# Optimization experiments

Hardware: AMD Instinct MI355X
Metric: run time of the kernel (lower is better)

Reference implementation:

```python
import jax, jax.numpy as jnp
import numpy as np

N, K, D = 131072, 1024, 10


def setup_inputs() -> dict:
    key = jax.random.key(0)
    k1, k2 = jax.random.split(key)
    encoder_embedding = jax.random.normal(k1, (N, D), dtype=jnp.float32)
    embedding_weight = jax.random.normal(k2, (K, D), dtype=jnp.float32)
    return {"encoder_embedding": encoder_embedding, "embedding_weight": embedding_weight}


def reference(encoder_embedding, embedding_weight):
    x = encoder_embedding            # [N, D]
    E = embedding_weight             # [K, D]
    x_sq = jnp.sum(x * x, axis=1, keepdims=True)          # [N, 1]
    e_sq = jnp.sum(E * E, axis=1)                         # [K]
    distance = x_sq + e_sq - 2.0 * jnp.einsum('nd,kd->nk', x, E)
    idx = jnp.argmin(distance, axis=1)                    # [N]
    quantized = E[idx]                                    # [N, D] gather
    # codebook (quantization) loss: mse(x.detach(), quantized)
    diff = jax.lax.stop_gradient(x) - quantized
    quantization_loss = jnp.mean(diff * diff)
    # straight-through estimator
    quantized_st = x + jax.lax.stop_gradient(quantized - x)
    return (quantized_st, quantization_loss)
```

## Files before the change

kernel.cpp:

```cpp
#include <hip/hip_runtime.h>


typedef __attribute__((ext_vector_type(8))) short short8;
typedef __attribute__((ext_vector_type(16))) float f32x16;

constexpr int N = 131072;
constexpr int K = 1024;
constexpr int D = 10;
constexpr int TILES = 32;
constexpr int THREADS = 512;
constexpr int BLOCKS = 256;
constexpr int ROWS_PER_WAVE = 64;
constexpr int AFRAG_N = TILES * 3 * 64;
constexpr int SMEM_A_BYTES = AFRAG_N * 16;
constexpr int SMEM_B_PER_WAVE = ROWS_PER_WAVE * 96;
constexpr int SMEM_BYTES = SMEM_A_BYTES + 8 * SMEM_B_PER_WAVE;

__device__ float4 g_afrag[AFRAG_N];

__device__ inline unsigned short f2bf(float f) {
    unsigned u = __float_as_uint(f);
    u += 0x7FFFu + ((u >> 16) & 1u);
    return (unsigned short)(u >> 16);
}
__device__ inline float bf2f(unsigned short h) {
    return __uint_as_float(((unsigned)h) << 16);
}

__global__ __launch_bounds__(256) void prep_afrag(const float* __restrict__ E) {
    const int gid = blockIdx.x * blockDim.x + threadIdx.x;
    if (gid >= AFRAG_N) return;
    const int tile = gid / 192;
    const int rem  = gid % 192;
    const int v    = rem / 64;
    const int L    = rem % 64;
    const int code = tile * 32 + (L & 31);
    const int h    = L >> 5;

    float e[D];
    #pragma unroll
    for (int d = 0; d < D; ++d) e[d] = E[code * D + d];
    float s = 0.f;
    #pragma unroll
    for (int d = 0; d < D; ++d) s = fmaf(e[d], e[d], s);
    const float ms = -0.5f * s;
    const unsigned short msh = f2bf(ms);
    const float r1 = ms - bf2f(msh);
    const unsigned short msm = f2bf(r1);
    const unsigned short msl = f2bf(r1 - bf2f(msm));

    unsigned short sl[8];
    #pragma unroll
    for (int i = 0; i < 8; ++i) {
        const int k = h * 8 + i;
        unsigned short o = 0;
        if (k < D) {
            const unsigned short eh = f2bf(e[k]);
            if (v == 0) o = eh;
            else {
                const float rm = e[k] - bf2f(eh);
                const unsigned short em = f2bf(rm);
                o = (v == 1) ? em : f2bf(rm - bf2f(em));
            }
        } else if (v == 0) {
            o = (k == 10) ? msh : (k == 11) ? msm : (k == 12) ? msl : (unsigned short)0;
        }
        sl[i] = o;
    }
    float4 w;
    unsigned* wp = (unsigned*)&w;
    #pragma unroll
    for (int q = 0; q < 4; ++q)
        wp[q] = (unsigned)sl[2 * q] | ((unsigned)sl[2 * q + 1] << 16);
    g_afrag[gid] = w;
}

__global__ __launch_bounds__(THREADS, 2) void vq_kernel(
    const float* __restrict__ x,
    const float* __restrict__ E,
    float* __restrict__ out,
    float* __restrict__ loss_out)
{
    extern __shared__ char smem[];
    float4* sA = (float4*)smem;
    char*   sB = smem + SMEM_A_BYTES;

    const int tid  = threadIdx.x;
    const int lane = tid & 63;
    const int wave = tid >> 6;
    const int rtW  = blockIdx.x * (BLOCKS ? (N / BLOCKS) : 0) + wave * ROWS_PER_WAVE;

    for (int i = tid; i < AFRAG_N; i += THREADS) sA[i] = g_afrag[i];

    {
        const float* xp = x + (size_t)(rtW + lane) * D;
        float xv[D];
        #pragma unroll
        for (int d = 0; d < D; d += 2) {
            float2 t2 = *reinterpret_cast<const float2*>(xp + d);
            xv[d] = t2.x; xv[d + 1] = t2.y;
        }
        unsigned short XH[D], XM[D], XL[D];
        #pragma unroll
        for (int d = 0; d < D; ++d) {
            XH[d] = f2bf(xv[d]); const float r1 = xv[d] - bf2f(XH[d]);
            XM[d] = f2bf(r1);    XL[d] = f2bf(r1 - bf2f(XM[d]));
        }
        unsigned short slots[48];
        #pragma unroll
        for (int s = 0; s < 16; ++s) {
            slots[s]      = (s < D) ? XH[s]
                          : (s <= 12 ? (unsigned short)0x3F80 : (unsigned short)0);
            slots[16 + s] = (s < D) ? XM[s] : (unsigned short)0;
            slots[32 + s] = (s < D) ? XL[s] : (unsigned short)0;
        }
        float4* bp = (float4*)(sB + wave * SMEM_B_PER_WAVE + lane * 96);
        #pragma unroll
        for (int q = 0; q < 6; ++q) {
            float4 w; unsigned* wp = (unsigned*)&w;
            #pragma unroll
            for (int p = 0; p < 4; ++p)
                wp[p] = (unsigned)slots[q * 8 + 2 * p] | ((unsigned)slots[q * 8 + 2 * p + 1] << 16);
            bp[q] = w;
        }
    }
    __syncthreads();

    const char* myB = sB + wave * SMEM_B_PER_WAVE;
    const int n   = lane & 31;
    const int h16 = (lane >> 5) * 16;
#define RDB(j, v) (*reinterpret_cast<const short8*>(myB + ((j) * 32 + n) * 96 + (v) * 32 + h16))
    const short8 b00 = RDB(0, 0), b01 = RDB(0, 1), b02 = RDB(0, 2);
    const short8 b10 = RDB(1, 0), b11 = RDB(1, 1), b12 = RDB(1, 2);
#undef RDB

    float best0 = -3.0e38f, best1 = -3.0e38f;
    int   bidx0 = 0,        bidx1 = 0;
    const int hibase = (lane >> 5) * 4;

    for (int t = 0; t < TILES; ++t) {
        const short8 a0 = *reinterpret_cast<const short8*>(&sA[(t * 3 + 0) * 64 + lane]);
        const short8 a1 = *reinterpret_cast<const short8*>(&sA[(t * 3 + 1) * 64 + lane]);
        const short8 a2 = *reinterpret_cast<const short8*>(&sA[(t * 3 + 2) * 64 + lane]);
        f32x16 c0, c1;
        #pragma unroll
        for (int i = 0; i < 16; ++i) { c0[i] = 0.f; c1[i] = 0.f; }
        c0 = __builtin_amdgcn_mfma_f32_32x32x16_bf16(a0, b00, c0, 0, 0, 0);
        c1 = __builtin_amdgcn_mfma_f32_32x32x16_bf16(a0, b10, c1, 0, 0, 0);
        c0 = __builtin_amdgcn_mfma_f32_32x32x16_bf16(a0, b01, c0, 0, 0, 0);
        c1 = __builtin_amdgcn_mfma_f32_32x32x16_bf16(a0, b11, c1, 0, 0, 0);
        c0 = __builtin_amdgcn_mfma_f32_32x32x16_bf16(a0, b02, c0, 0, 0, 0);
        c1 = __builtin_amdgcn_mfma_f32_32x32x16_bf16(a0, b12, c1, 0, 0, 0);
        c0 = __builtin_amdgcn_mfma_f32_32x32x16_bf16(a1, b00, c0, 0, 0, 0);
        c1 = __builtin_amdgcn_mfma_f32_32x32x16_bf16(a1, b10, c1, 0, 0, 0);
        c0 = __builtin_amdgcn_mfma_f32_32x32x16_bf16(a1, b01, c0, 0, 0, 0);
        c1 = __builtin_amdgcn_mfma_f32_32x32x16_bf16(a1, b11, c1, 0, 0, 0);
        c0 = __builtin_amdgcn_mfma_f32_32x32x16_bf16(a2, b00, c0, 0, 0, 0);
        c1 = __builtin_amdgcn_mfma_f32_32x32x16_bf16(a2, b10, c1, 0, 0, 0);

        const int tb = t * 32 + hibase;
        #pragma unroll
        for (int r = 0; r < 16; ++r) {
            const int ci = tb + ((r & 3) + 8 * (r >> 2));
            const bool g0 = c0[r] > best0;
            bidx0 = g0 ? ci : bidx0;  best0 = g0 ? c0[r] : best0;
            const bool g1 = c1[r] > best1;
            bidx1 = g1 ? ci : bidx1;  best1 = g1 ? c1[r] : best1;
        }
    }

    {
        float pb = __shfl_xor(best0, 32, 64);
        int   pi = __shfl_xor(bidx0, 32, 64);
        bool take = (pb > best0) || (pb == best0 && pi < bidx0);
        best0 = take ? pb : best0;  bidx0 = take ? pi : bidx0;
        pb = __shfl_xor(best1, 32, 64);
        pi = __shfl_xor(bidx1, 32, 64);
        take = (pb > best1) || (pb == best1 && pi < bidx1);
        best1 = take ? pb : best1;  bidx1 = take ? pi : bidx1;
    }

    const int   bi = (lane >> 5) ? bidx1 : bidx0;
    const float* ep = E   + (size_t)bi * D;
    const float* xp = x   + (size_t)(rtW + lane) * D;
    float*       op = out + (size_t)(rtW + lane) * D;
    float lsum = 0.f;
    #pragma unroll
    for (int d = 0; d < D; d += 2) {
        float2 ev = *reinterpret_cast<const float2*>(ep + d);
        float2 xw = *reinterpret_cast<const float2*>(xp + d);
        const float d0 = xw.x - ev.x, d1 = xw.y - ev.y;
        lsum = fmaf(d0, d0, lsum);  lsum = fmaf(d1, d1, lsum);
        float2 o;
        o.x = xw.x + (ev.x - xw.x);
        o.y = xw.y + (ev.y - xw.y);
        *reinterpret_cast<float2*>(op + d) = o;
    }
    #pragma unroll
    for (int off = 32; off > 0; off >>= 1)
        lsum += __shfl_down(lsum, off, 64);
    if (lane == 0)
        atomicAdd(loss_out, lsum * (1.0f / ((float)N * (float)D)));
}

extern "C" void kernel_launch(void* const* d_in, const int* in_sizes, int n_in,
                              void* d_out, int out_size, void* d_ws, size_t ws_size,
                              hipStream_t stream) {
    const float* x = (const float*)d_in[0];
    const float* E = (const float*)d_in[1];
    float* out  = (float*)d_out;
    float* loss = out + (size_t)N * D;

    hipMemsetAsync(loss, 0, sizeof(float), stream);
    prep_afrag<<<dim3(AFRAG_N / 256), dim3(256), 0, stream>>>(E);
    hipFuncSetAttribute((const void*)vq_kernel,
                        hipFuncAttributeMaxDynamicSharedMemorySize, SMEM_BYTES);
    vq_kernel<<<dim3(BLOCKS), dim3(THREADS), SMEM_BYTES, stream>>>(x, E, out, loss);
}
```

Measured before the change: 109.6 us.

## Keep codebook fragments in registers, split codes across waves, reduce argmin via LDS

Each wave now holds four codebook tiles (its slice of the codes) in registers instead of copying the whole codebook into LDS, and the block walks 32-row groups of inputs shared by all eight waves. Per-wave argmin results go to LDS and are merged by 32 threads, which also write the output and build the next group's B fragment. This removes the large per-block LDS codebook copy and allows more blocks per CU. In exchange it adds two block barriers per group, and only 32 threads do the gather, output and next-row prep while the rest wait, so the work is more serialized.

```diff
diff --git a/kernel.cpp b/kernel.cpp
--- a/kernel.cpp
+++ b/kernel.cpp
@@ -9,12 +9,11 @@
 constexpr int D = 10;
 constexpr int TILES = 32;
 constexpr int THREADS = 512;
-constexpr int BLOCKS = 256;
-constexpr int ROWS_PER_WAVE = 64;
+constexpr int BLOCKS = 512;
+constexpr int GROUPS = 8;
+constexpr int RPG = 32;
+constexpr int TPW = 4;
 constexpr int AFRAG_N = TILES * 3 * 64;
-constexpr int SMEM_A_BYTES = AFRAG_N * 16;
-constexpr int SMEM_B_PER_WAVE = ROWS_PER_WAVE * 96;
-constexpr int SMEM_BYTES = SMEM_A_BYTES + 8 * SMEM_B_PER_WAVE;
 
 __device__ float4 g_afrag[AFRAG_N];
 
@@ -75,132 +74,159 @@
     g_afrag[gid] = w;
 }
 
-__global__ __launch_bounds__(THREADS, 2) void vq_kernel(
+__device__ inline void build_b_row(const float* __restrict__ x, int grow,
+                                   int row, short8* __restrict__ sB) {
+    const float* xp = x + (size_t)grow * D;
+    float xv[D];
+    #pragma unroll
+    for (int d = 0; d < D; d += 2) {
+        float2 t2 = *reinterpret_cast<const float2*>(xp + d);
+        xv[d] = t2.x; xv[d + 1] = t2.y;
+    }
+    unsigned short XH[D], XM[D], XL[D];
+    #pragma unroll
+    for (int d = 0; d < D; ++d) {
+        XH[d] = f2bf(xv[d]); const float r1 = xv[d] - bf2f(XH[d]);
+        XM[d] = f2bf(r1);    XL[d] = f2bf(r1 - bf2f(XM[d]));
+    }
+    unsigned short slots[48];
+    #pragma unroll
+    for (int s = 0; s < 16; ++s) {
+        slots[s]      = (s < D) ? XH[s]
+                      : (s <= 12 ? (unsigned short)0x3F80 : (unsigned short)0);
+        slots[16 + s] = (s < D) ? XM[s] : (unsigned short)0;
+        slots[32 + s] = (s < D) ? XL[s] : (unsigned short)0;
+    }
+    #pragma unroll
+    for (int v = 0; v < 3; ++v)
+        #pragma unroll
+        for (int h = 0; h < 2; ++h) {
+            short8 w;
+            #pragma unroll
+            for (int i = 0; i < 8; ++i) w[i] = (short)slots[v * 16 + h * 8 + i];
+            sB[(v * 2 + h) * 32 + row] = w;
+        }
+}
+
+#define MFMA __builtin_amdgcn_mfma_f32_32x32x16_bf16
+
+__global__ __launch_bounds__(THREADS, 4) void vq_kernel(
     const float* __restrict__ x,
     const float* __restrict__ E,
     float* __restrict__ out,
     float* __restrict__ loss_out)
 {
-    extern __shared__ char smem[];
-    float4* sA = (float4*)smem;
-    char*   sB = smem + SMEM_A_BYTES;
+    __shared__ short8 sB[6 * 32];
+    __shared__ float  sScore[8][RPG];
+    __shared__ int    sIdx[8][RPG];
 
     const int tid  = threadIdx.x;
     const int lane = tid & 63;
     const int wave = tid >> 6;
-    const int rtW  = blockIdx.x * (BLOCKS ? (N / BLOCKS) : 0) + wave * ROWS_PER_WAVE;
-
-    for (int i = tid; i < AFRAG_N; i += THREADS) sA[i] = g_afrag[i];
-
-    {
-        const float* xp = x + (size_t)(rtW + lane) * D;
-        float xv[D];
-        #pragma unroll
-        for (int d = 0; d < D; d += 2) {
-            float2 t2 = *reinterpret_cast<const float2*>(xp + d);
-            xv[d] = t2.x; xv[d + 1] = t2.y;
-        }
-        unsigned short XH[D], XM[D], XL[D];
-        #pragma unroll
-        for (int d = 0; d < D; ++d) {
-            XH[d] = f2bf(xv[d]); const float r1 = xv[d] - bf2f(XH[d]);
-            XM[d] = f2bf(r1);    XL[d] = f2bf(r1 - bf2f(XM[d]));
-        }
-        unsigned short slots[48];
-        #pragma unroll
-        for (int s = 0; s < 16; ++s) {
-            slots[s]      = (s < D) ? XH[s]
-                          : (s <= 12 ? (unsigned short)0x3F80 : (unsigned short)0);
-            slots[16 + s] = (s < D) ? XM[s] : (unsigned short)0;
-            slots[32 + s] = (s < D) ? XL[s] : (unsigned short)0;
-        }
-        float4* bp = (float4*)(sB + wave * SMEM_B_PER_WAVE + lane * 96);
-        #pragma unroll
-        for (int q = 0; q < 6; ++q) {
-            float4 w; unsigned* wp = (unsigned*)&w;
-            #pragma unroll
-            for (int p = 0; p < 4; ++p)
-                wp[p] = (unsigned)slots[q * 8 + 2 * p] | ((unsigned)slots[q * 8 + 2 * p + 1] << 16);
-            bp[q] = w;
-        }
-    }
+    const int n    = lane & 31;
+    const int hf   = lane >> 5;
+    const int hibase = hf * 4;
+    const int wtile  = wave * TPW;
+    const int blockRow = blockIdx.x * (GROUPS * RPG);
+
+    const short8* ga = (const short8*)g_afrag;
+    short8 a[TPW][3];
+    #pragma unroll
+    for (int t = 0; t < TPW; ++t)
+        #pragma unroll
+        for (int v = 0; v < 3; ++v)
+            a[t][v] = ga[((wtile + t) * 3 + v) * 64 + lane];
+
+    if (tid < RPG) build_b_row(x, blockRow + tid, tid, sB);
     __syncthreads();
 
-    const char* myB = sB + wave * SMEM_B_PER_WAVE;
-    const int n   = lane & 31;
-    const int h16 = (lane >> 5) * 16;
-#define RDB(j, v) (*reinterpret_cast<const short8*>(myB + ((j) * 32 + n) * 96 + (v) * 32 + h16))
-    const short8 b00 = RDB(0, 0), b01 = RDB(0, 1), b02 = RDB(0, 2);
-    const short8 b10 = RDB(1, 0), b11 = RDB(1, 1), b12 = RDB(1, 2);
-#undef RDB
-
-    float best0 = -3.0e38f, best1 = -3.0e38f;
-    int   bidx0 = 0,        bidx1 = 0;
-    const int hibase = (lane >> 5) * 4;
-
-    for (int t = 0; t < TILES; ++t) {
-        const short8 a0 = *reinterpret_cast<const short8*>(&sA[(t * 3 + 0) * 64 + lane]);
-        const short8 a1 = *reinterpret_cast<const short8*>(&sA[(t * 3 + 1) * 64 + lane]);
-        const short8 a2 = *reinterpret_cast<const short8*>(&sA[(t * 3 + 2) * 64 + lane]);
-        f32x16 c0, c1;
-        #pragma unroll
-        for (int i = 0; i < 16; ++i) { c0[i] = 0.f; c1[i] = 0.f; }
-        c0 = __builtin_amdgcn_mfma_f32_32x32x16_bf16(a0, b00, c0, 0, 0, 0);
-        c1 = __builtin_amdgcn_mfma_f32_32x32x16_bf16(a0, b10, c1, 0, 0, 0);
-        c0 = __builtin_amdgcn_mfma_f32_32x32x16_bf16(a0, b01, c0, 0, 0, 0);
-        c1 = __builtin_amdgcn_mfma_f32_32x32x16_bf16(a0, b11, c1, 0, 0, 0);
-        c0 = __builtin_amdgcn_mfma_f32_32x32x16_bf16(a0, b02, c0, 0, 0, 0);
-        c1 = __builtin_amdgcn_mfma_f32_32x32x16_bf16(a0, b12, c1, 0, 0, 0);
-        c0 = __builtin_amdgcn_mfma_f32_32x32x16_bf16(a1, b00, c0, 0, 0, 0);
-        c1 = __builtin_amdgcn_mfma_f32_32x32x16_bf16(a1, b10, c1, 0, 0, 0);
-        c0 = __builtin_amdgcn_mfma_f32_32x32x16_bf16(a1, b01, c0, 0, 0, 0);
-        c1 = __builtin_amdgcn_mfma_f32_32x32x16_bf16(a1, b11, c1, 0, 0, 0);
-        c0 = __builtin_amdgcn_mfma_f32_32x32x16_bf16(a2, b00, c0, 0, 0, 0);
-        c1 = __builtin_amdgcn_mfma_f32_32x32x16_bf16(a2, b10, c1, 0, 0, 0);
-
-        const int tb = t * 32 + hibase;
-        #pragma unroll
-        for (int r = 0; r < 16; ++r) {
-            const int ci = tb + ((r & 3) + 8 * (r >> 2));
-            const bool g0 = c0[r] > best0;
-            bidx0 = g0 ? ci : bidx0;  best0 = g0 ? c0[r] : best0;
-            const bool g1 = c1[r] > best1;
-            bidx1 = g1 ? ci : bidx1;  best1 = g1 ? c1[r] : best1;
-        }
-    }
-
-    {
-        float pb = __shfl_xor(best0, 32, 64);
-        int   pi = __shfl_xor(bidx0, 32, 64);
-        bool take = (pb > best0) || (pb == best0 && pi < bidx0);
-        best0 = take ? pb : best0;  bidx0 = take ? pi : bidx0;
-        pb = __shfl_xor(best1, 32, 64);
-        pi = __shfl_xor(bidx1, 32, 64);
-        take = (pb > best1) || (pb == best1 && pi < bidx1);
-        best1 = take ? pb : best1;  bidx1 = take ? pi : bidx1;
-    }
-
-    const int   bi = (lane >> 5) ? bidx1 : bidx0;
-    const float* ep = E   + (size_t)bi * D;
-    const float* xp = x   + (size_t)(rtW + lane) * D;
-    float*       op = out + (size_t)(rtW + lane) * D;
     float lsum = 0.f;
-    #pragma unroll
-    for (int d = 0; d < D; d += 2) {
-        float2 ev = *reinterpret_cast<const float2*>(ep + d);
-        float2 xw = *reinterpret_cast<const float2*>(xp + d);
-        const float d0 = xw.x - ev.x, d1 = xw.y - ev.y;
-        lsum = fmaf(d0, d0, lsum);  lsum = fmaf(d1, d1, lsum);
-        float2 o;
-        o.x = xw.x + (ev.x - xw.x);
-        o.y = xw.y + (ev.y - xw.y);
-        *reinterpret_cast<float2*>(op + d) = o;
-    }
-    #pragma unroll
-    for (int off = 32; off > 0; off >>= 1)
-        lsum += __shfl_down(lsum, off, 64);
-    if (lane == 0)
-        atomicAdd(loss_out, lsum * (1.0f / ((float)N * (float)D)));
+
+    for (int g = 0; g < GROUPS; ++g) {
+        const int rowBase = blockRow + g * RPG;
+
+        const short8 b0 = sB[(0 * 2 + hf) * 32 + n];
+        const short8 b1 = sB[(1 * 2 + hf) * 32 + n];
+        const short8 b2 = sB[(2 * 2 + hf) * 32 + n];
+
+        float best = -3.0e38f;
+        int   lci  = 0;
+
+        #pragma unroll
+        for (int p = 0; p < TPW / 2; ++p) {
+            const int t0 = 2 * p, t1 = 2 * p + 1;
+            f32x16 c0, c1;
+            #pragma unroll
+            for (int i = 0; i < 16; ++i) { c0[i] = 0.f; c1[i] = 0.f; }
+            c0 = MFMA(a[t0][0], b0, c0, 0, 0, 0);  c1 = MFMA(a[t1][0], b0, c1, 0, 0, 0);
+            c0 = MFMA(a[t0][0], b1, c0, 0, 0, 0);  c1 = MFMA(a[t1][0], b1, c1, 0, 0, 0);
+            c0 = MFMA(a[t0][0], b2, c0, 0, 0, 0);  c1 = MFMA(a[t1][0], b2, c1, 0, 0, 0);
+            c0 = MFMA(a[t0][1], b0, c0, 0, 0, 0);  c1 = MFMA(a[t1][1], b0, c1, 0, 0, 0);
+            c0 = MFMA(a[t0][1], b1, c0, 0, 0, 0);  c1 = MFMA(a[t1][1], b1, c1, 0, 0, 0);
+            c0 = MFMA(a[t0][2], b0, c0, 0, 0, 0);  c1 = MFMA(a[t1][2], b0, c1, 0, 0, 0);
+
+            #pragma unroll
+            for (int r = 0; r < 16; ++r) {
+                const bool gt = c0[r] > best;
+                lci  = gt ? (t0 * 16 + r) : lci;
+                best = fmaxf(best, c0[r]);
+            }
+            #pragma unroll
+            for (int r = 0; r < 16; ++r) {
+                const bool gt = c1[r] > best;
+                lci  = gt ? (t1 * 16 + r) : lci;
+                best = fmaxf(best, c1[r]);
+            }
+        }
+
+        const int tt = lci >> 4, rr = lci & 15;
+        int bidx = (wtile + tt) * 32 + hibase + ((rr & 3) + 8 * (rr >> 2));
+
+        {
+            const float pb = __shfl_xor(best, 32, 64);
+            const int   pi = __shfl_xor(bidx, 32, 64);
+            const bool take = (pb > best) || (pb == best && pi < bidx);
+            best = take ? pb : best;  bidx = take ? pi : bidx;
+        }
+        if (lane < 32) { sScore[wave][n] = best; sIdx[wave][n] = bidx; }
+        __syncthreads();
+
+        if (tid < RPG) {
+            float bs = sScore[0][tid];
+            int   bi = sIdx[0][tid];
+            #pragma unroll
+            for (int w = 1; w < 8; ++w) {
+                const float s  = sScore[w][tid];
+                const int   i2 = sIdx[w][tid];
+                if (s > bs) { bs = s; bi = i2; }
+            }
+            const float* ep = E   + (size_t)bi * D;
+            const float* xp = x   + (size_t)(rowBase + tid) * D;
+            float*       op = out + (size_t)(rowBase + tid) * D;
+            #pragma unroll
+            for (int d = 0; d < D; d += 2) {
+                float2 ev = *reinterpret_cast<const float2*>(ep + d);
+                float2 xw = *reinterpret_cast<const float2*>(xp + d);
+                const float d0 = xw.x - ev.x, d1 = xw.y - ev.y;
+                lsum = fmaf(d0, d0, lsum);  lsum = fmaf(d1, d1, lsum);
+                float2 o;
+                o.x = xw.x + (ev.x - xw.x);
+                o.y = xw.y + (ev.y - xw.y);
+                *reinterpret_cast<float2*>(op + d) = o;
+            }
+            if (g + 1 < GROUPS)
+                build_b_row(x, rowBase + RPG + tid, tid, sB);
+        }
+        __syncthreads();
+    }
+
+    if (tid < 64) {
+        #pragma unroll
+        for (int off = 32; off > 0; off >>= 1)
+            lsum += __shfl_down(lsum, off, 64);
+        if (tid == 0)
+            atomicAdd(loss_out, lsum * (1.0f / ((float)N * (float)D)));
+    }
 }
 
 extern "C" void kernel_launch(void* const* d_in, const int* in_sizes, int n_in,
@@ -213,7 +239,5 @@
 
     hipMemsetAsync(loss, 0, sizeof(float), stream);
     prep_afrag<<<dim3(AFRAG_N / 256), dim3(256), 0, stream>>>(E);
-    hipFuncSetAttribute((const void*)vq_kernel,
-                        hipFuncAttributeMaxDynamicSharedMemorySize, SMEM_BYTES);
-    vq_kernel<<<dim3(BLOCKS), dim3(THREADS), SMEM_BYTES, stream>>>(x, E, out, loss);
-}
+    vq_kernel<<<dim3(BLOCKS), dim3(THREADS), 0, stream>>>(x, E, out, loss);
+}
```

Result: faster. 93.49 us (-14.7%).
